# Kernel tuning notes

Hardware: AMD Instinct MI355X
Metric: run time of the kernel (lower is better)

## Reference

```python
import jax, jax.numpy as jnp
import numpy as np

B, C, OC, K, HW = 32, 256, 256, 3, 56
M, G = 2, 2
GAP = max(16, C // 16)          # input_gap = 16
MO = M * OC                      # fc1 out channels = 512
FC2_OUT = OC * C * K * K         # 589824
PER = FC2_OUT // MO              # per-group out channels of fc2 = 1152


def setup_inputs() -> dict:
    key = jax.random.key(0)
    ks = jax.random.split(key, 6)
    x = jax.random.normal(ks[0], (B, C, HW, HW), dtype=jnp.float32)
    reduce_w = jax.random.normal(ks[1], (GAP, C), dtype=jnp.float32) / np.sqrt(C)
    reduce_b = jnp.zeros((GAP,), dtype=jnp.float32)
    fc1_w = jax.random.normal(ks[2], (MO, GAP), dtype=jnp.float32) / np.sqrt(GAP)
    # fc2: grouped 1x1 conv, groups=G*OC=512, 1 in-channel per group -> weight (FC2_OUT,)
    fc2_w = jax.random.normal(ks[3], (FC2_OUT,), dtype=jnp.float32)
    fc2_b = jax.random.normal(ks[4], (FC2_OUT,), dtype=jnp.float32) * 0.01
    return {"x": x, "reduce_w": reduce_w, "reduce_b": reduce_b,
            "fc1_w": fc1_w, "fc2_w": fc2_w, "fc2_b": fc2_b}


def reference(x, reduce_w, reduce_b, fc1_w, fc2_w, fc2_b):
    b, c, h, w = x.shape
    # global average pool -> (b, C)
    gap = x.mean(axis=(2, 3))
    # reduce: 1x1 conv on 1x1 map == linear
    g = gap @ reduce_w.T + reduce_b                      # (b, GAP)
    # fc1 (no bias) + sigmoid
    a = jax.nn.sigmoid(g @ fc1_w.T)                      # (b, MO)
    # fc2: grouped 1x1 conv with 1 input channel per group:
    # out[:, g*PER + j] = a[:, g] * fc2_w[g*PER + j] + fc2_b[g*PER + j]
    wk = a[:, :, None] * fc2_w.reshape(MO, PER)[None] + fc2_b.reshape(MO, PER)[None]
    wk = wk.reshape(b * OC, c, K, K)                     # per-sample conv kernels
    pad = K // 2
    y = jax.lax.conv_general_dilated(
        x.reshape(1, b * c, h, w), wk,
        window_strides=(1, 1), padding=[(pad, pad), (pad, pad)],
        feature_group_count=b,
        dimension_numbers=("NCHW", "OIHW", "NCHW"))
    return y.reshape(b, OC, y.shape[2], y.shape[3])
```

## Files before the change

### kernel.cpp

```cpp
#include <hip/hip_runtime.h>
#include <hip/hip_bf16.h>
#include <stdint.h>

#define NB   32
#define NC   256
#define NOC  256
#define HWD  56
#define NPIX 3136
#define PW   58
#define PPIX 3364
#define KTOT 2304
#define MOD  512
#define GAPD 16

#define XBT_BYTES ((size_t)NB * PPIX * NC * 2)
#define WA_BYTES  ((size_t)NB * NOC * KTOT * 2)

typedef __bf16 bf16x8 __attribute__((ext_vector_type(8)));
typedef float  f32x4  __attribute__((ext_vector_type(4)));
typedef unsigned short u16x8 __attribute__((ext_vector_type(8)));

__device__ __forceinline__ unsigned short f2bf(float f) {
    union { float f; unsigned int u; } v; v.f = f;
    unsigned int u = v.u;
    return (unsigned short)((u + 0x7FFFu + ((u >> 16) & 1u)) >> 16);
}

__global__ void se_kernel(const float* __restrict__ gap,
                          const float* __restrict__ rw, const float* __restrict__ rb,
                          const float* __restrict__ f1w, float* __restrict__ a2) {
    __shared__ float sgap[NB * NC];
    __shared__ float sg[NB * GAPD];
    int t = threadIdx.x;
    #pragma unroll
    for (int i = 0; i < 16; ++i) sgap[i * 512 + t] = gap[i * 512 + t];
    __syncthreads();
    {
        int b = t >> 4, tt = t & 15;
        float s = rb[tt];
        for (int c = 0; c < NC; ++c) s += sgap[b * NC + c] * rw[tt * NC + c];
        sg[b * GAPD + tt] = s;
    }
    __syncthreads();
    for (int i = 0; i < 32; ++i) {
        int o = i * 512 + t;
        int b = o >> 9, m = o & 511;
        float s = 0.f;
        #pragma unroll
        for (int tt = 0; tt < GAPD; ++tt) s += sg[b * GAPD + tt] * f1w[m * GAPD + tt];
        a2[o] = 1.0f / (1.0f + __expf(-s));
    }
}

__global__ void wk_kernel(const float* __restrict__ a2,
                          const float* __restrict__ f2w, const float* __restrict__ f2b,
                          unsigned short* __restrict__ wa) {
    __shared__ float sw[KTOT];
    __shared__ float sbv[KTOT];
    int oc = blockIdx.x, b = blockIdx.y, c = threadIdx.x;
    const float4* wsrc = (const float4*)(f2w + (size_t)oc * KTOT);
    const float4* bsrc = (const float4*)(f2b + (size_t)oc * KTOT);
    #pragma unroll
    for (int i = 0; i < 3; ++i) {
        int idx = i * 256 + c;
        if (idx < 576) {
            float4 wv = wsrc[idx], bv = bsrc[idx];
            ((float4*)sw)[idx] = wv;
            ((float4*)sbv)[idx] = bv;
        }
    }
    float a0 = a2[b * MOD + 2 * oc];
    float a1 = a2[b * MOD + 2 * oc + 1];
    __syncthreads();
    unsigned short* dst = wa + (size_t)(b * NOC + oc) * KTOT;
    #pragma unroll
    for (int s = 0; s < 9; ++s) {
        int rem = c * 9 + s;
        float a = (rem >= 1152) ? a1 : a0;
        float v = a * sw[rem] + sbv[rem];
        dst[s * NC + c] = f2bf(v);
    }
}

__global__ void halo_kernel(unsigned short* __restrict__ xbt) {
    int b = blockIdx.x, t = threadIdx.x;
    unsigned short* xb = xbt + (size_t)b * PPIX * NC;
    u16x8 z = {};
    for (int i = t; i < 3712; i += 256) {
        int r = (i >= 1856) ? 1 : 0;
        int c = i - r * 1856;
        int pix = r * (57 * 58) + (c >> 5);
        *(u16x8*)(xb + (size_t)pix * NC + (c & 31) * 8) = z;
    }
    for (int i = t; i < 3584; i += 256) {
        int row = 1 + (i >> 6);
        int side = (i >> 5) & 1;
        int pix = row * PW + side * 57;
        *(u16x8*)(xb + (size_t)pix * NC + (i & 31) * 8) = z;
    }
}

#define TSTR 59
__global__ void xpose_kernel(const float* __restrict__ x, unsigned short* __restrict__ xbt,
                             float* __restrict__ gap) {
    __shared__ unsigned short tile[NC * TSTR];
    int py = blockIdx.x, b = blockIdx.y, t = threadIdx.x;
    int wv = t >> 6, l = t & 63;
    const float* xs = x + (size_t)b * NC * NPIX + py * HWD;
    int q = l & 15;
    int rb4 = l >> 4;
    #pragma unroll
    for (int it = 0; it < 16; ++it) {
        int c = wv * 64 + it * 4 + rb4;
        if (q < 14) {
            float4 v = *(const float4*)(xs + (size_t)c * NPIX + q * 4);
            unsigned short* tr = tile + c * TSTR + q * 4;
            tr[0] = f2bf(v.x); tr[1] = f2bf(v.y); tr[2] = f2bf(v.z); tr[3] = f2bf(v.w);
        }
    }
    __syncthreads();
    {
        float s = 0.f;
        #pragma unroll
        for (int px = 0; px < 56; ++px) {
            union { unsigned int u; float f; } cv;
            cv.u = ((unsigned int)tile[t * TSTR + px]) << 16;
            s += cv.f;
        }
        atomicAdd(&gap[b * NC + t], s * (1.0f / NPIX));
    }
    int cch = t & 31, pg = t >> 5;
    for (int i = 0; i < 7; ++i) {
        int px = pg * 7 + i;
        u16x8 v;
        #pragma unroll
        for (int j = 0; j < 8; ++j) v[j] = tile[(cch * 8 + j) * TSTR + px];
        *(u16x8*)(xbt + ((size_t)b * PPIX + (size_t)(1 + py) * PW + 1 + px) * NC + cch * 8) = v;
    }
}

#define SLICE_BYTES 32768
#define B_OFF 16384

#define PWAIT(N) do { asm volatile("s_waitcnt vmcnt(" #N ")" ::: "memory"); \
    __builtin_amdgcn_s_barrier(); __builtin_amdgcn_sched_barrier(0); } while (0)

__global__ __launch_bounds__(256, 1) void conv_gemm(
    const unsigned short* __restrict__ wa,
    const unsigned short* __restrict__ xbt,
    float* __restrict__ out)
{
    __shared__ __attribute__((aligned(16))) char lds[4 * SLICE_BYTES];

    const int bid = blockIdx.x;
    const int wg  = (bid & 7) * 52 + (bid >> 3);
    const int nt  = wg % 13, b = wg / 13;

    const int t = threadIdx.x;
    const int w = t >> 6, l = t & 63;
    const int wm = w >> 1, wn = w & 1;

    const unsigned short* waB = wa + (size_t)b * NOC * KTOT;
    const unsigned short* xbB = xbt + (size_t)b * PPIX * NC;

    const int srow = l >> 2;
    const int sq   = (l & 3) ^ ((l >> 3) & 3);
    const unsigned short* pA[4];
    const unsigned short* pB[4];
    #pragma unroll
    for (int i = 0; i < 4; ++i) {
        int m = i * 64 + w * 16 + srow;
        pA[i] = waB + (size_t)m * KTOT + sq * 8;
        int pg = nt * 256 + m; if (pg > NPIX - 1) pg = NPIX - 1;
        int py = pg / 56, px = pg - py * 56;
        pB[i] = xbB + (size_t)((py + 1) * PW + (px + 1)) * NC + sq * 8;
    }

    f32x4 acc[8][8] = {};

    auto issue = [&](int tp) {
        char* sb = lds + (tp & 3) * SLICE_BYTES;
        const int koff = tp * 32;
        const int s9 = tp >> 3;
        const int dy = s9 / 3, dx = s9 - dy * 3;
        const int bsh = ((dy - 1) * PW + (dx - 1)) * NC + (tp & 7) * 32;
        #pragma unroll
        for (int i = 0; i < 4; ++i)
            __builtin_amdgcn_global_load_lds(
                (const __attribute__((address_space(1))) void*)(pA[i] + koff),
                (__attribute__((address_space(3))) void*)(sb + (i * 4 + w) * 1024), 16, 0, 0);
        #pragma unroll
        for (int i = 0; i < 4; ++i)
            __builtin_amdgcn_global_load_lds(
                (const __attribute__((address_space(1))) void*)(pB[i] + bsh),
                (__attribute__((address_space(3))) void*)(sb + B_OFF + (i * 4 + w) * 1024), 16, 0, 0);
    };

    const int physq16 = (((l >> 4) ^ ((l >> 1) & 3)) << 4);
    const int arow = (l & 15) << 6;

    auto compute = [&](int p) {
        const char* sb = lds + (p & 3) * SLICE_BYTES;
        bf16x8 af[8], bfr[8];
        #pragma unroll
        for (int i = 0; i < 8; ++i)
            af[i] = *(const bf16x8*)(sb + wm * 8192 + i * 1024 + arow + physq16);
        #pragma unroll
        for (int j = 0; j < 8; ++j)
            bfr[j] = *(const bf16x8*)(sb + B_OFF + wn * 8192 + j * 1024 + arow + physq16);
        __builtin_amdgcn_s_setprio(1);
        #pragma unroll
        for (int i = 0; i < 8; ++i)
            #pragma unroll
            for (int j = 0; j < 8; ++j)
                acc[i][j] = __builtin_amdgcn_mfma_f32_16x16x32_bf16(af[i], bfr[j], acc[i][j], 0, 0, 0);
        __builtin_amdgcn_s_setprio(0);
    };

    issue(0); issue(1);
    #pragma unroll 4
    for (int p = 0; p < 68; ++p) { issue(p + 2); PWAIT(16); compute(p); }
    issue(70); PWAIT(16); compute(68);
    issue(71); PWAIT(16); compute(69);
    PWAIT(8);  compute(70);
    PWAIT(0);  compute(71);

    const int ocb = wm * 128 + ((l >> 4) << 2);
    const int pxb = nt * 256 + wn * 128 + (l & 15);
    #pragma unroll
    for (int i = 0; i < 8; ++i) {
        #pragma unroll
        for (int j = 0; j < 8; ++j) {
            int p = pxb + j * 16;
            if (p < NPIX) {
                float* o = out + ((size_t)(b * NOC + ocb + i * 16)) * NPIX + p;
                o[0]        = acc[i][j][0];
                o[NPIX]     = acc[i][j][1];
                o[2 * NPIX] = acc[i][j][2];
                o[3 * NPIX] = acc[i][j][3];
            }
        }
    }
}

extern "C" void kernel_launch(void* const* d_in, const int* in_sizes, int n_in,
                              void* d_out, int out_size, void* d_ws, size_t ws_size,
                              hipStream_t stream) {
    (void)in_sizes; (void)n_in; (void)out_size; (void)ws_size;
    const float* x   = (const float*)d_in[0];
    const float* rw  = (const float*)d_in[1];
    const float* rb  = (const float*)d_in[2];
    const float* f1w = (const float*)d_in[3];
    const float* f2w = (const float*)d_in[4];
    const float* f2b = (const float*)d_in[5];
    float* out = (float*)d_out;

    char* wsb = (char*)d_ws;
    unsigned short* xbt = (unsigned short*)wsb;
    unsigned short* wa  = (unsigned short*)(wsb + XBT_BYTES);
    float* gap = (float*)(wsb + XBT_BYTES + WA_BYTES);
    float* a2  = (float*)(wsb + XBT_BYTES + WA_BYTES + (size_t)NB * NC * 4);

    hipMemsetAsync(gap, 0, (size_t)NB * NC * 4, stream);
    halo_kernel<<<dim3(32), 256, 0, stream>>>(xbt);
    xpose_kernel<<<dim3(56, 32), 256, 0, stream>>>(x, xbt, gap);
    se_kernel<<<dim3(1), 512, 0, stream>>>(gap, rw, rb, f1w, a2);
    wk_kernel<<<dim3(256, 32), 256, 0, stream>>>(a2, f2w, f2b, wa);
    conv_gemm<<<dim3(416), 256, 0, stream>>>(wa, xbt, out);
}
```

Measured before the change: 223.5 us.

## Restructure conv GEMM to 8 waves with 9-slot LDS ring and interleaved staging

The implicit-GEMM conv kernel moves from 4 waves per block to 8 waves (2x4), and each wave's tile shrinks from 128x128 to 128x64. The LDS layout becomes a ring of nine 16 KB half-slices, K steps grow from 32 to 64, and the swizzle changes to an 8-way XOR. Global-to-LDS loads are issued one half-slice at a time inside the MFMA sub-steps so that loads overlap compute more finely. In exchange the kernel uses more barriers per tile and more LDS (144 KB), so only one block fits per CU despite the launch bound asking for two, and the added synchronization may stall waves.

```diff
diff --git a/kernel.cpp b/kernel.cpp
--- a/kernel.cpp
+++ b/kernel.cpp
@@ -139,18 +139,16 @@
     }
 }
 
-#define SLICE_BYTES 32768
-#define B_OFF 16384
-
-#define PWAIT(N) do { asm volatile("s_waitcnt vmcnt(" #N ")" ::: "memory"); \
-    __builtin_amdgcn_s_barrier(); __builtin_amdgcn_sched_barrier(0); } while (0)
-
-__global__ __launch_bounds__(256, 1) void conv_gemm(
+#define SLOT 16384
+#define NSLOT 9
+#define NHALF 144
+
+__global__ __launch_bounds__(512, 2) void conv_gemm(
     const unsigned short* __restrict__ wa,
     const unsigned short* __restrict__ xbt,
     float* __restrict__ out)
 {
-    __shared__ __attribute__((aligned(16))) char lds[4 * SLICE_BYTES];
+    __shared__ __attribute__((aligned(16))) char lds[NSLOT * SLOT];
 
     const int bid = blockIdx.x;
     const int wg  = (bid & 7) * 52 + (bid >> 3);
@@ -158,79 +156,111 @@
 
     const int t = threadIdx.x;
     const int w = t >> 6, l = t & 63;
-    const int wm = w >> 1, wn = w & 1;
+    const int wm = w >> 2, wn = w & 3;
 
     const unsigned short* waB = wa + (size_t)b * NOC * KTOT;
     const unsigned short* xbB = xbt + (size_t)b * PPIX * NC;
 
-    const int srow = l >> 2;
-    const int sq   = (l & 3) ^ ((l >> 3) & 3);
-    const unsigned short* pA[4];
-    const unsigned short* pB[4];
+    const int srow = t >> 3;
+    const int sq8  = ((t & 7) ^ (srow & 7)) * 8;
+    const unsigned short* pA0 = waB + (size_t)srow * KTOT + sq8;
+    const unsigned short* pBr[4];
     #pragma unroll
     for (int i = 0; i < 4; ++i) {
-        int m = i * 64 + w * 16 + srow;
-        pA[i] = waB + (size_t)m * KTOT + sq * 8;
-        int pg = nt * 256 + m; if (pg > NPIX - 1) pg = NPIX - 1;
+        int pg = nt * 256 + i * 64 + srow; if (pg > NPIX - 1) pg = NPIX - 1;
         int py = pg / 56, px = pg - py * 56;
-        pB[i] = xbB + (size_t)((py + 1) * PW + (px + 1)) * NC + sq * 8;
-    }
-
-    f32x4 acc[8][8] = {};
-
-    auto issue = [&](int tp) {
-        char* sb = lds + (tp & 3) * SLICE_BYTES;
-        const int koff = tp * 32;
-        const int s9 = tp >> 3;
-        const int dy = s9 / 3, dx = s9 - dy * 3;
-        const int bsh = ((dy - 1) * PW + (dx - 1)) * NC + (tp & 7) * 32;
-        #pragma unroll
-        for (int i = 0; i < 4; ++i)
+        pBr[i] = xbB + (size_t)((py + 1) * PW + (px + 1)) * NC + sq8;
+    }
+
+    auto stage = [&](int h, int slot) {
+        const int kt = h >> 2, j = h & 3;
+        char* sb = lds + slot * SLOT;
+        __attribute__((address_space(3))) void* d1 =
+            (__attribute__((address_space(3))) void*)(sb + t * 16);
+        __attribute__((address_space(3))) void* d2 =
+            (__attribute__((address_space(3))) void*)(sb + 8192 + t * 16);
+        if (j < 2) {
+            const unsigned short* s1 = pA0 + (size_t)(j * 128) * KTOT + kt * 64;
             __builtin_amdgcn_global_load_lds(
-                (const __attribute__((address_space(1))) void*)(pA[i] + koff),
-                (__attribute__((address_space(3))) void*)(sb + (i * 4 + w) * 1024), 16, 0, 0);
-        #pragma unroll
-        for (int i = 0; i < 4; ++i)
+                (const __attribute__((address_space(1))) void*)s1, d1, 16, 0, 0);
             __builtin_amdgcn_global_load_lds(
-                (const __attribute__((address_space(1))) void*)(pB[i] + bsh),
-                (__attribute__((address_space(3))) void*)(sb + B_OFF + (i * 4 + w) * 1024), 16, 0, 0);
+                (const __attribute__((address_space(1))) void*)(s1 + (size_t)64 * KTOT), d2, 16, 0, 0);
+        } else {
+            const int s9 = kt >> 2;
+            const int dy = (s9 >= 6) ? 2 : ((s9 >= 3) ? 1 : 0);
+            const int dx = s9 - dy * 3;
+            const int bsh = ((dy - 1) * PW + (dx - 1)) * NC + (kt & 3) * 64;
+            const unsigned short* s1 = pBr[(j - 2) * 2] + bsh;
+            const unsigned short* s2 = pBr[(j - 2) * 2 + 1] + bsh;
+            __builtin_amdgcn_global_load_lds(
+                (const __attribute__((address_space(1))) void*)s1, d1, 16, 0, 0);
+            __builtin_amdgcn_global_load_lds(
+                (const __attribute__((address_space(1))) void*)s2, d2, 16, 0, 0);
+        }
     };
 
-    const int physq16 = (((l >> 4) ^ ((l >> 1) & 3)) << 4);
-    const int arow = (l & 15) << 6;
-
-    auto compute = [&](int p) {
-        const char* sb = lds + (p & 3) * SLICE_BYTES;
-        bf16x8 af[8], bfr[8];
-        #pragma unroll
-        for (int i = 0; i < 8; ++i)
-            af[i] = *(const bf16x8*)(sb + wm * 8192 + i * 1024 + arow + physq16);
-        #pragma unroll
-        for (int j = 0; j < 8; ++j)
-            bfr[j] = *(const bf16x8*)(sb + B_OFF + wn * 8192 + j * 1024 + arow + physq16);
-        __builtin_amdgcn_s_setprio(1);
-        #pragma unroll
-        for (int i = 0; i < 8; ++i)
+    const int laneA = (l & 15) * 128;
+    const int laneQ0 = (((0 * 4 + (l >> 4)) ^ (l & 7)) << 4);
+    const int laneQ1 = (((1 * 4 + (l >> 4)) ^ (l & 7)) << 4);
+
+    f32x4 acc[8][4] = {};
+    bf16x8 af[8];
+
+    #pragma unroll
+    for (int h = 0; h < 5; ++h) stage(h, h);
+    asm volatile("s_waitcnt vmcnt(2)" ::: "memory");
+    __builtin_amdgcn_s_barrier();
+    __builtin_amdgcn_sched_barrier(0);
+
+    int slotC = 0;
+    int hS = 5;
+    int slotS = 5;
+
+    for (int T = 0; T < 36; ++T) {
+        int sA = slotC + wm;             if (sA >= NSLOT) sA -= NSLOT;
+        int sB = slotC + 2 + (wn >> 1);  if (sB >= NSLOT) sB -= NSLOT;
+        const char* Abase = lds + sA * SLOT + laneA;
+        const char* Bbase = lds + sB * SLOT + (wn & 1) * 8192 + laneA;
+
+        #pragma unroll
+        for (int q = 0; q < 4; ++q) {
+            const int laneQ = (q >> 1) ? laneQ1 : laneQ0;
+            const int np = q & 1;
+            if (q == 0 || q == 2) {
+                #pragma unroll
+                for (int m = 0; m < 8; ++m)
+                    af[m] = *(const bf16x8*)(Abase + m * 2048 + laneQ);
+            }
+            bf16x8 bf0 = *(const bf16x8*)(Bbase + (np * 2) * 2048 + laneQ);
+            bf16x8 bf1 = *(const bf16x8*)(Bbase + (np * 2 + 1) * 2048 + laneQ);
+            if (hS < NHALF) stage(hS, slotS);
+            ++hS; ++slotS; if (slotS >= NSLOT) slotS -= NSLOT;
+
+            __builtin_amdgcn_s_barrier();
+            asm volatile("s_waitcnt lgkmcnt(0)" ::: "memory");
+            __builtin_amdgcn_sched_barrier(0);
+            __builtin_amdgcn_s_setprio(1);
             #pragma unroll
-            for (int j = 0; j < 8; ++j)
-                acc[i][j] = __builtin_amdgcn_mfma_f32_16x16x32_bf16(af[i], bfr[j], acc[i][j], 0, 0, 0);
-        __builtin_amdgcn_s_setprio(0);
-    };
-
-    issue(0); issue(1);
-    #pragma unroll 4
-    for (int p = 0; p < 68; ++p) { issue(p + 2); PWAIT(16); compute(p); }
-    issue(70); PWAIT(16); compute(68);
-    issue(71); PWAIT(16); compute(69);
-    PWAIT(8);  compute(70);
-    PWAIT(0);  compute(71);
+            for (int m = 0; m < 8; ++m) {
+                acc[m][np * 2]     = __builtin_amdgcn_mfma_f32_16x16x32_bf16(af[m], bf0, acc[m][np * 2], 0, 0, 0);
+                acc[m][np * 2 + 1] = __builtin_amdgcn_mfma_f32_16x16x32_bf16(af[m], bf1, acc[m][np * 2 + 1], 0, 0, 0);
+            }
+            __builtin_amdgcn_s_setprio(0);
+            if (q < 3) __builtin_amdgcn_s_barrier();
+        }
+        if (T < 34)       asm volatile("s_waitcnt vmcnt(2)" ::: "memory");
+        else if (T == 34) asm volatile("s_waitcnt vmcnt(0)" ::: "memory");
+        __builtin_amdgcn_s_barrier();
+        __builtin_amdgcn_sched_barrier(0);
+        slotC += 4; if (slotC >= NSLOT) slotC -= NSLOT;
+    }
 
     const int ocb = wm * 128 + ((l >> 4) << 2);
-    const int pxb = nt * 256 + wn * 128 + (l & 15);
+    const int pxb = nt * 256 + wn * 64 + (l & 15);
     #pragma unroll
     for (int i = 0; i < 8; ++i) {
         #pragma unroll
-        for (int j = 0; j < 8; ++j) {
+        for (int j = 0; j < 4; ++j) {
             int p = pxb + j * 16;
             if (p < NPIX) {
                 float* o = out + ((size_t)(b * NOC + ocb + i * 16)) * NPIX + p;
@@ -266,5 +296,5 @@
     xpose_kernel<<<dim3(56, 32), 256, 0, stream>>>(x, xbt, gap);
     se_kernel<<<dim3(1), 512, 0, stream>>>(gap, rw, rb, f1w, a2);
     wk_kernel<<<dim3(256, 32), 256, 0, stream>>>(a2, f2w, f2b, wa);
-    conv_gemm<<<dim3(416), 256, 0, stream>>>(wa, xbt, out);
-}
+    conv_gemm<<<dim3(416), 512, 0, stream>>>(wa, xbt, out);
+}
```

Measured after the change: 208.4 us. 6.8% less time.

## Retile conv GEMM to 256x160 with 3-stage pipeline and two blocks per CU

Applied to the files above, without the earlier changes.

The implicit-GEMM conv kernel changes its pixel tile from 256 to 160. This raises the grid from 416 to 640 blocks, which balances better across CUs. LDS buffering drops from 4 slots to 3, launch bounds allow 2 blocks per CU, and the LDS swizzle/load mapping is rebuilt for the new tile shape. Separately, the wk_kernel now loops over all batch samples per block, reusing the loaded fc2 weights instead of reloading them per sample. The trade-offs are a shallower prefetch pipeline, lower MFMA reuse per loaded A tile, and more register pressure with two resident blocks.

```diff
diff --git a/kernel.cpp b/kernel.cpp
--- a/kernel.cpp
+++ b/kernel.cpp
@@ -57,29 +57,34 @@
                           unsigned short* __restrict__ wa) {
     __shared__ float sw[KTOT];
     __shared__ float sbv[KTOT];
-    int oc = blockIdx.x, b = blockIdx.y, c = threadIdx.x;
+    __shared__ float sa[2 * NB];
+    int oc = blockIdx.x, c = threadIdx.x;
     const float4* wsrc = (const float4*)(f2w + (size_t)oc * KTOT);
     const float4* bsrc = (const float4*)(f2b + (size_t)oc * KTOT);
     #pragma unroll
     for (int i = 0; i < 3; ++i) {
         int idx = i * 256 + c;
         if (idx < 576) {
-            float4 wv = wsrc[idx], bv = bsrc[idx];
-            ((float4*)sw)[idx] = wv;
-            ((float4*)sbv)[idx] = bv;
-        }
-    }
-    float a0 = a2[b * MOD + 2 * oc];
-    float a1 = a2[b * MOD + 2 * oc + 1];
+            ((float4*)sw)[idx] = wsrc[idx];
+            ((float4*)sbv)[idx] = bsrc[idx];
+        }
+    }
+    if (c < 64) sa[c] = a2[(c >> 1) * MOD + 2 * oc + (c & 1)];
     __syncthreads();
-    unsigned short* dst = wa + (size_t)(b * NOC + oc) * KTOT;
-    #pragma unroll
-    for (int s = 0; s < 9; ++s) {
-        int rem = c * 9 + s;
-        float a = (rem >= 1152) ? a1 : a0;
-        float v = a * sw[rem] + sbv[rem];
-        dst[s * NC + c] = f2bf(v);
-    }
+    float w9[9], b9[9];
+    #pragma unroll
+    for (int s = 0; s < 9; ++s) { w9[s] = sw[c * 9 + s]; b9[s] = sbv[c * 9 + s]; }
+    bool hi = (c * 9 + 8) >= 1152;
+    for (int b = 0; b < NB; ++b) {
+        float a0 = sa[2 * b], a1 = sa[2 * b + 1];
+        unsigned short* dst = wa + (size_t)(b * NOC + oc) * KTOT;
+        #pragma unroll
+        for (int s = 0; s < 9; ++s) {
+            float a = ((c * 9 + s) >= 1152) ? a1 : a0;
+            dst[s * NC + c] = f2bf(a * w9[s] + b9[s]);
+        }
+    }
+    (void)hi;
 }
 
 __global__ void halo_kernel(unsigned short* __restrict__ xbt) {
@@ -139,22 +144,20 @@
     }
 }
 
-#define SLICE_BYTES 32768
-#define B_OFF 16384
-
-#define PWAIT(N) do { asm volatile("s_waitcnt vmcnt(" #N ")" ::: "memory"); \
-    __builtin_amdgcn_s_barrier(); __builtin_amdgcn_sched_barrier(0); } while (0)
-
-__global__ __launch_bounds__(256, 1) void conv_gemm(
+#define SLICE 26624
+#define BOFF  16384
+#define PXT   160
+
+__global__ __launch_bounds__(256, 2) void conv_gemm(
     const unsigned short* __restrict__ wa,
     const unsigned short* __restrict__ xbt,
     float* __restrict__ out)
 {
-    __shared__ __attribute__((aligned(16))) char lds[4 * SLICE_BYTES];
+    __shared__ __attribute__((aligned(16))) char lds[3 * SLICE];
 
     const int bid = blockIdx.x;
-    const int wg  = (bid & 7) * 52 + (bid >> 3);
-    const int nt  = wg % 13, b = wg / 13;
+    const int wg  = (bid & 7) * 80 + (bid >> 3);
+    const int b   = wg / 20, nt = wg % 20;
 
     const int t = threadIdx.x;
     const int w = t >> 6, l = t & 63;
@@ -163,74 +166,117 @@
     const unsigned short* waB = wa + (size_t)b * NOC * KTOT;
     const unsigned short* xbB = xbt + (size_t)b * PPIX * NC;
 
-    const int srow = l >> 2;
-    const int sq   = (l & 3) ^ ((l >> 3) & 3);
-    const unsigned short* pA[4];
-    const unsigned short* pB[4];
+    const unsigned short* srcA[4];
     #pragma unroll
     for (int i = 0; i < 4; ++i) {
-        int m = i * 64 + w * 16 + srow;
-        pA[i] = waB + (size_t)m * KTOT + sq * 8;
-        int pg = nt * 256 + m; if (pg > NPIX - 1) pg = NPIX - 1;
+        int e = i * 4 + w;
+        int s = e * 64 + l;
+        int u = s >> 3, p3 = s & 7;
+        int d = p3 ^ (u & 7);
+        int kq = d >> 1, sub = d & 1;
+        int row = 2 * u + sub;
+        srcA[i] = waB + (size_t)row * KTOT + kq * 8;
+    }
+    const unsigned short* srcB[3];
+    int actB[3];
+    #pragma unroll
+    for (int i = 0; i < 3; ++i) {
+        int e = (i + 4) * 4 + w;
+        actB[i] = (e < 26);
+        int s = (e - 16) * 64 + l;
+        if (s > 639) s = 639;
+        int u = s >> 3, p3 = s & 7;
+        int d = p3 ^ (u & 7);
+        int kq = d >> 1, sub = d & 1;
+        int prow = 2 * u + sub;
+        int pg = nt * PXT + prow; if (pg > NPIX - 1) pg = NPIX - 1;
         int py = pg / 56, px = pg - py * 56;
-        pB[i] = xbB + (size_t)((py + 1) * PW + (px + 1)) * NC + sq * 8;
-    }
-
-    f32x4 acc[8][8] = {};
-
-    auto issue = [&](int tp) {
-        char* sb = lds + (tp & 3) * SLICE_BYTES;
-        const int koff = tp * 32;
+        srcB[i] = xbB + (size_t)((py + 1) * PW + (px + 1)) * NC + kq * 8;
+    }
+    const int l16 = l * 16;
+
+    auto issue = [&](int tp, int slot) {
+        char* sb = lds + slot * SLICE;
         const int s9 = tp >> 3;
-        const int dy = s9 / 3, dx = s9 - dy * 3;
+        const int dy = (s9 >= 6) ? 2 : ((s9 >= 3) ? 1 : 0);
+        const int dx = s9 - dy * 3;
         const int bsh = ((dy - 1) * PW + (dx - 1)) * NC + (tp & 7) * 32;
         #pragma unroll
-        for (int i = 0; i < 4; ++i)
+        for (int i = 0; i < 4; ++i) {
+            int e = i * 4 + w;
             __builtin_amdgcn_global_load_lds(
-                (const __attribute__((address_space(1))) void*)(pA[i] + koff),
-                (__attribute__((address_space(3))) void*)(sb + (i * 4 + w) * 1024), 16, 0, 0);
-        #pragma unroll
-        for (int i = 0; i < 4; ++i)
-            __builtin_amdgcn_global_load_lds(
-                (const __attribute__((address_space(1))) void*)(pB[i] + bsh),
-                (__attribute__((address_space(3))) void*)(sb + B_OFF + (i * 4 + w) * 1024), 16, 0, 0);
+                (const __attribute__((address_space(1))) void*)(srcA[i] + tp * 32),
+                (__attribute__((address_space(3))) void*)(sb + e * 1024 + l16), 16, 0, 0);
+        }
+        #pragma unroll
+        for (int i = 0; i < 3; ++i) {
+            if (actB[i]) {
+                int e = (i + 4) * 4 + w;
+                __builtin_amdgcn_global_load_lds(
+                    (const __attribute__((address_space(1))) void*)(srcB[i] + bsh),
+                    (__attribute__((address_space(3))) void*)(sb + e * 1024 + l16), 16, 0, 0);
+            }
+        }
     };
 
-    const int physq16 = (((l >> 4) ^ ((l >> 1) & 3)) << 4);
-    const int arow = (l & 15) << 6;
-
-    auto compute = [&](int p) {
-        const char* sb = lds + (p & 3) * SLICE_BYTES;
-        bf16x8 af[8], bfr[8];
-        #pragma unroll
-        for (int i = 0; i < 8; ++i)
-            af[i] = *(const bf16x8*)(sb + wm * 8192 + i * 1024 + arow + physq16);
-        #pragma unroll
-        for (int j = 0; j < 8; ++j)
-            bfr[j] = *(const bf16x8*)(sb + B_OFF + wn * 8192 + j * 1024 + arow + physq16);
+    const int subq = ((l >> 4) << 1) | (l & 1);
+    const int ulow = (l >> 1) & 7;
+    const int aoff0 = (wm * 64 + ((l & 15) >> 1)) * 128 + ((subq ^ ulow) << 4);
+    const int boff0 = BOFF + (wn * 40 + ((l & 15) >> 1)) * 128 + ((subq ^ ulow) << 4);
+
+    f32x4 acc[8][5] = {};
+
+    issue(0, 0); issue(1, 1);
+
+    int cs = 0, is2 = 2;
+    for (int p = 0; p < 71; ++p) {
+        asm volatile("s_waitcnt vmcnt(6)" ::: "memory");
+        __builtin_amdgcn_s_barrier();
+        __builtin_amdgcn_sched_barrier(0);
+        if (p < 70) {
+            issue(p + 2, is2);
+            ++is2; if (is2 == 3) is2 = 0;
+        }
+        const char* sb = lds + cs * SLICE;
+        ++cs; if (cs == 3) cs = 0;
+        bf16x8 af[8];
+        #pragma unroll
+        for (int m = 0; m < 8; ++m)
+            af[m] = *(const bf16x8*)(sb + aoff0 + m * 1024);
         __builtin_amdgcn_s_setprio(1);
         #pragma unroll
-        for (int i = 0; i < 8; ++i)
+        for (int j = 0; j < 5; ++j) {
+            bf16x8 bf = *(const bf16x8*)(sb + boff0 + j * 1024);
             #pragma unroll
-            for (int j = 0; j < 8; ++j)
-                acc[i][j] = __builtin_amdgcn_mfma_f32_16x16x32_bf16(af[i], bfr[j], acc[i][j], 0, 0, 0);
+            for (int m = 0; m < 8; ++m)
+                acc[m][j] = __builtin_amdgcn_mfma_f32_16x16x32_bf16(af[m], bf, acc[m][j], 0, 0, 0);
+        }
         __builtin_amdgcn_s_setprio(0);
-    };
-
-    issue(0); issue(1);
-    #pragma unroll 4
-    for (int p = 0; p < 68; ++p) { issue(p + 2); PWAIT(16); compute(p); }
-    issue(70); PWAIT(16); compute(68);
-    issue(71); PWAIT(16); compute(69);
-    PWAIT(8);  compute(70);
-    PWAIT(0);  compute(71);
+    }
+    asm volatile("s_waitcnt vmcnt(0)" ::: "memory");
+    __builtin_amdgcn_s_barrier();
+    __builtin_amdgcn_sched_barrier(0);
+    {
+        const char* sb = lds + cs * SLICE;
+        bf16x8 af[8];
+        #pragma unroll
+        for (int m = 0; m < 8; ++m)
+            af[m] = *(const bf16x8*)(sb + aoff0 + m * 1024);
+        #pragma unroll
+        for (int j = 0; j < 5; ++j) {
+            bf16x8 bf = *(const bf16x8*)(sb + boff0 + j * 1024);
+            #pragma unroll
+            for (int m = 0; m < 8; ++m)
+                acc[m][j] = __builtin_amdgcn_mfma_f32_16x16x32_bf16(af[m], bf, acc[m][j], 0, 0, 0);
+        }
+    }
 
     const int ocb = wm * 128 + ((l >> 4) << 2);
-    const int pxb = nt * 256 + wn * 128 + (l & 15);
+    const int pxb = nt * PXT + wn * 80 + (l & 15);
     #pragma unroll
     for (int i = 0; i < 8; ++i) {
         #pragma unroll
-        for (int j = 0; j < 8; ++j) {
+        for (int j = 0; j < 5; ++j) {
             int p = pxb + j * 16;
             if (p < NPIX) {
                 float* o = out + ((size_t)(b * NOC + ocb + i * 16)) * NPIX + p;
@@ -265,6 +311,6 @@
     halo_kernel<<<dim3(32), 256, 0, stream>>>(xbt);
     xpose_kernel<<<dim3(56, 32), 256, 0, stream>>>(x, xbt, gap);
     se_kernel<<<dim3(1), 512, 0, stream>>>(gap, rw, rb, f1w, a2);
-    wk_kernel<<<dim3(256, 32), 256, 0, stream>>>(a2, f2w, f2b, wa);
-    conv_gemm<<<dim3(416), 256, 0, stream>>>(wa, xbt, out);
-}
+    wk_kernel<<<dim3(256), 256, 0, stream>>>(a2, f2w, f2b, wa);
+    conv_gemm<<<dim3(640), 256, 0, stream>>>(wa, xbt, out);
+}
```

Measured after the change: 219.0 us. 2.0% less time.
